# Performance work log

Hardware: AMD Instinct MI355X
Metric: run time of the kernel (lower is better)

Reference implementation:

```python
import jax, jax.numpy as jnp
import numpy as np

L, N, E, D = 4, 50000, 250000, 128
EPS = 1e-5

def _ln(h, g, b):
    mu = jnp.mean(h, axis=-1, keepdims=True)
    var = jnp.mean(jnp.square(h - mu), axis=-1, keepdims=True)
    return (h - mu) * jax.lax.rsqrt(var + EPS) * g + b

def setup_inputs() -> dict:
    key = jax.random.key(0)
    ks = jax.random.split(key, 8)
    s1 = 1.0 / np.sqrt(3 * D)
    s2 = 1.0 / np.sqrt(D)
    s3 = 1.0 / np.sqrt(2 * D)
    return {
        "x": jax.random.normal(ks[0], (N, D), jnp.float32),
        "edge_index": jax.random.randint(ks[1], (2, E), 0, N, jnp.int32),
        "edge_attr": jax.random.normal(ks[2], (E, D), jnp.float32),
        "eW1": jax.random.normal(ks[3], (L, 3 * D, D), jnp.float32) * s1,
        "eb1": jnp.zeros((L, D), jnp.float32),
        "eW2": jax.random.normal(ks[4], (L, D, D), jnp.float32) * s2,
        "eb2": jnp.zeros((L, D), jnp.float32),
        "eG": jnp.ones((L, D), jnp.float32),
        "eB": jnp.zeros((L, D), jnp.float32),
        "nW1": jax.random.normal(ks[5], (L, 2 * D, D), jnp.float32) * s3,
        "nb1": jnp.zeros((L, D), jnp.float32),
        "nW2": jax.random.normal(ks[6], (L, D, D), jnp.float32) * s2,
        "nb2": jnp.zeros((L, D), jnp.float32),
        "nG": jnp.ones((L, D), jnp.float32),
        "nB": jnp.zeros((L, D), jnp.float32),
    }

def reference(x, edge_index, edge_attr, eW1, eb1, eW2, eb2, eG, eB,
              nW1, nb1, nW2, nb2, nG, nB):
    src = edge_index[0]  # scatter target (custom aggregate uses edge_index[0])
    dst = edge_index[1]  # x_i under PyG source_to_target flow
    n_nodes = x.shape[0]

    def step(carry, p):
        xc, ea = carry
        ew1, eb1_, ew2, eb2_, eg, ebt, nw1, nb1_, nw2, nb2_, ng, nbt = p
        # message: cat(x_i, x_j, edge_attr) -> MLP -> residual
        m = jnp.concatenate([xc[dst], xc[src], ea], axis=1)  # [E, 3D]
        h = jax.nn.relu(m @ ew1 + eb1_) @ ew2 + eb2_
        ea_new = ea + _ln(h, eg, ebt)
        # aggregate: scatter-sum edges into nodes by edge_index[0]
        agg = jax.ops.segment_sum(ea_new, src, num_segments=n_nodes)  # [N, D]
        # update: cat(x, agg) -> MLP -> residual
        u = jnp.concatenate([xc, agg], axis=1)  # [N, 2D]
        h2 = jax.nn.relu(u @ nw1 + nb1_) @ nw2 + nb2_
        x_new = xc + _ln(h2, ng, nbt)
        return (x_new, ea_new), None

    (x_out, ea_out), _ = jax.lax.scan(
        step, (x, edge_attr),
        (eW1, eb1, eW2, eb2, eG, eB, nW1, nb1, nW2, nb2, nG, nB))
    return x_out, ea_out
```

## Files before the change

### kernel.cpp

```cpp
#include <hip/hip_runtime.h>
#include <hip/hip_bf16.h>

#define N_NODES 50000
#define N_EDGES 250000
#define DIM 128
#define LAYERS 4
#define LN_EPS 1e-5f

typedef __hip_bfloat16 bf16;
typedef float f32x4 __attribute__((ext_vector_type(4)));
typedef __bf16 bfx8 __attribute__((ext_vector_type(8)));
typedef unsigned short u16x8 __attribute__((ext_vector_type(8)));
typedef unsigned short u16x4 __attribute__((ext_vector_type(4)));
typedef unsigned int   u32x4 __attribute__((ext_vector_type(4)));

#define F_X   0
#define F_EA  1
#define F_EW1 2
#define F_EW2 3
#define F_EG  4
#define F_NW1 5
#define F_NW2 6
#define F_NG  7

__device__ __forceinline__ float b2f(bf16 v) { return __bfloat162float(v); }
__device__ __forceinline__ bf16  f2b(float v) { return __float2bfloat16(v); }
__device__ __forceinline__ unsigned short f2us(float v) {
    return __builtin_bit_cast(unsigned short, __float2bfloat16(v));
}
__device__ __forceinline__ float us2f(unsigned short u) {
    return __builtin_bit_cast(float, (unsigned)u << 16);
}

__device__ __forceinline__ float ldv(const void* p, size_t i, int f) {
    if (f) return ((const float*)p)[i];
    else   return b2f(((const bf16*)p)[i]);
}
__device__ __forceinline__ void stv(void* p, size_t i, float v, int f) {
    if (f) ((float*)p)[i] = v;
    else   ((bf16*)p)[i] = f2b(v);
}

__device__ __forceinline__ bfx8 cvt8(f32x4 lo, f32x4 hi) {
    u16x8 u;
    #pragma unroll
    for (int i = 0; i < 4; i++) { u[i] = f2us(lo[i]); u[i + 4] = f2us(hi[i]); }
    return __builtin_bit_cast(bfx8, u);
}

__device__ __forceinline__ void mfma8(const bf16* pBk, bfx8 a, f32x4* acc) {
    #pragma unroll
    for (int f = 0; f < 8; f++) {
        bfx8 b = *reinterpret_cast<const bfx8*>(pBk + f * 128);
        acc[f] = __builtin_amdgcn_mfma_f32_16x16x32_bf16(a, b, acc[f], 0, 0, 0);
    }
}

__global__ void k_detect(const void* x, const void* ea,
                         const void* eW1, const void* eW2,
                         const void* nW1, const void* nW2,
                         const void* eG, const void* nG,
                         int* flags)
{
    __shared__ int bad[6];
    const void* ptrs[6] = { x, ea, eW1, eW2, nW1, nW2 };
    const int t = threadIdx.x;
    if (t < 6) bad[t] = 0;
    __syncthreads();
    for (int b = 0; b < 6; b++) {
        const bf16* p = (const bf16*)ptrs[b];
        int isbad = 0;
        for (int i = t; i < 4096; i += 256) {
            float v = b2f(p[i]);
            if (!(fabsf(v) < 1e4f)) isbad = 1;
        }
        if (isbad) atomicOr(&bad[b], 1);
    }
    __syncthreads();
    if (t == 0) {
        flags[F_X]   = bad[0];
        flags[F_EA]  = bad[1];
        flags[F_EW1] = bad[2];
        flags[F_EW2] = bad[3];
        flags[F_NW1] = bad[4];
        flags[F_NW2] = bad[5];
        const bf16* g1 = (const bf16*)eG;
        const bf16* g2 = (const bf16*)nG;
        flags[F_EG] = (b2f(g1[0]) == 1.0f && b2f(g1[1]) == 1.0f) ? 0 : 1;
        flags[F_NG] = (b2f(g2[0]) == 1.0f && b2f(g2[1]) == 1.0f) ? 0 : 1;
    }
}

__global__ void k_init_x(const void* __restrict__ x_in, float* __restrict__ xf,
                         bf16* __restrict__ xb, const int* __restrict__ flags) {
    const int f = flags[F_X];
    size_t i = ((size_t)blockIdx.x * 256 + threadIdx.x) * 4;
    if (i >= (size_t)N_NODES * DIM) return;
    f32x4 v;
    if (f) {
        v = *(const f32x4*)((const float*)x_in + i);
    } else {
        u16x4 u = *(const u16x4*)((const unsigned short*)x_in + i);
        #pragma unroll
        for (int q = 0; q < 4; q++) v[q] = us2f(u[q]);
    }
    *(f32x4*)(xf + i) = v;
    u16x4 ub;
    #pragma unroll
    for (int q = 0; q < 4; q++) ub[q] = f2us(v[q]);
    *(u16x4*)((unsigned short*)xb + i) = ub;
}

__global__ void k_init_ea(const void* __restrict__ ea_in, void* __restrict__ d_out,
                          const int* __restrict__ flags) {
    const int fe = flags[F_EA];
    const int fo = flags[F_X];
    size_t i = ((size_t)blockIdx.x * 256 + threadIdx.x) * 4;
    if (i >= (size_t)N_EDGES * DIM) return;
    if (fe == fo) {
        if (fo) {
            float* d = (float*)d_out + (size_t)N_NODES * DIM;
            *(u32x4*)(d + i) = *(const u32x4*)((const float*)ea_in + i);
        } else {
            bf16* d = (bf16*)d_out + (size_t)N_NODES * DIM;
            *(u16x4*)((unsigned short*)d + i) =
                *(const u16x4*)((const unsigned short*)ea_in + i);
        }
    } else {
        f32x4 v;
        if (fe) v = *(const f32x4*)((const float*)ea_in + i);
        else {
            u16x4 u = *(const u16x4*)((const unsigned short*)ea_in + i);
            #pragma unroll
            for (int q = 0; q < 4; q++) v[q] = us2f(u[q]);
        }
        if (fo) {
            float* d = (float*)d_out + (size_t)N_NODES * DIM;
            *(f32x4*)(d + i) = v;
        } else {
            bf16* d = (bf16*)d_out + (size_t)N_NODES * DIM;
            u16x4 ub;
            #pragma unroll
            for (int q = 0; q < 4; q++) ub[q] = f2us(v[q]);
            *(u16x4*)((unsigned short*)d + i) = ub;
        }
    }
}

__global__ void k_wprep(const void* __restrict__ W, bf16* __restrict__ Wb,
                        int K, const int* __restrict__ flags, int fidx)
{
    const int f = flags[fidx];
    size_t i = (size_t)blockIdx.x * 256 + threadIdx.x;
    const int per = K * DIM;
    if (i >= (size_t)LAYERS * per) return;
    int l   = (int)(i / per);
    int rem = (int)(i % per);
    int j   = rem & 7;
    int c   = (rem >> 3) & 127;
    int kq  = rem >> 10;
    int k   = kq * 8 + j;
    Wb[i] = f2b(ldv(W, (size_t)l * per + (size_t)k * DIM + c, f));
}

__global__ void k_deg(const int* __restrict__ srcI, int* __restrict__ deg) {
    int e = blockIdx.x * 256 + threadIdx.x;
    if (e < N_EDGES) atomicAdd(&deg[srcI[e]], 1);
}

#define SCH ((N_NODES + 255) / 256)
__global__ void k_scan(const int* __restrict__ deg, int* __restrict__ off,
                       int* __restrict__ cur) {
    __shared__ int part[256];
    const int t = threadIdx.x;
    const int lo = t * SCH;
    const int hi = (lo + SCH < N_NODES) ? (lo + SCH) : N_NODES;
    int s = 0;
    for (int i = lo; i < hi; i++) s += deg[i];
    part[t] = s;
    __syncthreads();
    if (t == 0) {
        int run = 0;
        for (int i = 0; i < 256; i++) { int v = part[i]; part[i] = run; run += v; }
    }
    __syncthreads();
    int run = part[t];
    for (int i = lo; i < hi; i++) { off[i] = run; cur[i] = run; run += deg[i]; }
    if (hi == N_NODES) off[N_NODES] = run;
}

__global__ void k_fill(const int* __restrict__ srcI, int* __restrict__ cur,
                       int* __restrict__ lst) {
    int e = blockIdx.x * 256 + threadIdx.x;
    if (e < N_EDGES) {
        int p = atomicAdd(&cur[srcI[e]], 1);
        lst[p] = e;
    }
}

__global__ __launch_bounds__(256)
void k_edge(const bf16* __restrict__ xb,
            void* __restrict__ d_out,
            const int* __restrict__ srcI, const int* __restrict__ dstI,
            const bf16* __restrict__ W1b, const bf16* __restrict__ W2b,
            const void* __restrict__ b1, const void* __restrict__ b2,
            const void* __restrict__ G,  const void* __restrict__ B,
            const int* __restrict__ flags, int layer)
{
    __shared__ alignas(16) float smem[4][16 * 132];

    const int fo = flags[F_X];
    const int fg = flags[F_EG];

    void* ea = fo ? (void*)((float*)d_out + (size_t)N_NODES * DIM)
                  : (void*)((bf16*)d_out + (size_t)N_NODES * DIM);

    const bf16* W1l = W1b + (size_t)layer * 3 * DIM * DIM;
    const bf16* W2l = W2b + (size_t)layer * DIM * DIM;
    const bf16* b1l = (const bf16*)b1 + (size_t)layer * DIM;
    const bf16* b2l = (const bf16*)b2 + (size_t)layer * DIM;
    const bf16* Bl  = (const bf16*)B  + (size_t)layer * DIM;
    const void* Gl  = fg ? (const void*)((const float*)G + (size_t)layer * DIM)
                         : (const void*)((const bf16*)G  + (size_t)layer * DIM);

    const int tid  = threadIdx.x;
    const int wv   = tid >> 6;
    const int lane = tid & 63;
    const int cl   = lane & 15;
    const int kp   = lane >> 4;

    const int e0w = blockIdx.x * 64 + wv * 16;
    const int eA  = (e0w + cl < N_EDGES) ? (e0w + cl) : (N_EDGES - 1);
    const bf16* pAd = xb + (size_t)dstI[eA] * DIM + kp * 8;
    const bf16* pAs = xb + (size_t)srcI[eA] * DIM + kp * 8;
    const bf16* pB  = W1l + kp * 1024 + cl * 8;

    f32x4 acc[8];
    #pragma unroll
    for (int f = 0; f < 8; f++) acc[f] = (f32x4){0.f, 0.f, 0.f, 0.f};

    #pragma unroll
    for (int kk = 0; kk < 4; kk++)
        mfma8(pB + (size_t)kk * 4096,
              *reinterpret_cast<const bfx8*>(pAd + kk * 32), acc);
    #pragma unroll
    for (int kk = 0; kk < 4; kk++)
        mfma8(pB + (size_t)(kk + 4) * 4096,
              *reinterpret_cast<const bfx8*>(pAs + kk * 32), acc);
    if (fo) {
        const float* pAe = (const float*)ea + (size_t)eA * DIM + kp * 8;
        #pragma unroll
        for (int kk = 0; kk < 4; kk++) {
            f32x4 lo = *reinterpret_cast<const f32x4*>(pAe + kk * 32);
            f32x4 hi = *reinterpret_cast<const f32x4*>(pAe + kk * 32 + 4);
            mfma8(pB + (size_t)(kk + 8) * 4096, cvt8(lo, hi), acc);
        }
    } else {
        const bf16* pAe = (const bf16*)ea + (size_t)eA * DIM + kp * 8;
        #pragma unroll
        for (int kk = 0; kk < 4; kk++)
            mfma8(pB + (size_t)(kk + 8) * 4096,
                  *reinterpret_cast<const bfx8*>(pAe + kk * 32), acc);
    }

    char* hb = (char*)&smem[wv][0];
    #pragma unroll
    for (int f = 0; f < 8; f++) {
        const int col = f * 16 + cl;
        const float bias1 = b2f(b1l[col]);
        #pragma unroll
        for (int j = 0; j < 4; j++) {
            const int r = kp * 4 + j;
            float hv = fmaxf(acc[f][j] + bias1, 0.f);
            *(bf16*)(hb + r * 256 + ((col * 2) ^ ((r & 7) << 4))) = f2b(hv);
        }
    }

    const bf16* pB2 = W2l + kp * 1024 + cl * 8;
    f32x4 acc2[8];
    #pragma unroll
    for (int f = 0; f < 8; f++) acc2[f] = (f32x4){0.f, 0.f, 0.f, 0.f};
    #pragma unroll
    for (int kk = 0; kk < 4; kk++) {
        bfx8 a = *reinterpret_cast<const bfx8*>(
            hb + cl * 256 + ((kk * 64 + kp * 16) ^ ((cl & 7) << 4)));
        mfma8(pB2 + (size_t)kk * 4096, a, acc2);
    }

    float g_[8], be_[8];
    #pragma unroll
    for (int f = 0; f < 8; f++) {
        const int col = f * 16 + cl;
        const float bias2 = b2f(b2l[col]);
        #pragma unroll
        for (int j = 0; j < 4; j++) acc2[f][j] += bias2;
        g_[f]  = ldv(Gl, col, fg);
        be_[f] = b2f(Bl[col]);
    }
    float mu[4], rs[4];
    #pragma unroll
    for (int j = 0; j < 4; j++) {
        float s = 0.f, q = 0.f;
        #pragma unroll
        for (int f = 0; f < 8; f++) { float v = acc2[f][j]; s += v; q += v * v; }
        #pragma unroll
        for (int m = 1; m <= 8; m <<= 1) { s += __shfl_xor(s, m); q += __shfl_xor(q, m); }
        mu[j] = s * (1.f / DIM);
        float var = q * (1.f / DIM) - mu[j] * mu[j];
        rs[j] = rsqrtf(var + LN_EPS);
    }

    float* vs = &smem[wv][0];
    #pragma unroll
    for (int f = 0; f < 8; f++) {
        #pragma unroll
        for (int j = 0; j < 4; j++) {
            const float val = (acc2[f][j] - mu[j]) * rs[j] * g_[f] + be_[f];
            vs[(kp * 4 + j) * 132 + f * 16 + cl] = val;
        }
    }
    const int lr = lane >> 5;
    const int lc = (lane & 31) * 4;
    #pragma unroll
    for (int i = 0; i < 8; i++) {
        const int r2 = 2 * i + lr;
        const int e  = e0w + r2;
        if (e >= N_EDGES) continue;
        f32x4 v = *(const f32x4*)&vs[r2 * 132 + lc];
        const size_t off = (size_t)e * DIM + lc;
        if (fo) {
            float* pe = (float*)ea + off;
            f32x4 o = *(const f32x4*)pe;
            *(f32x4*)pe = o + v;
        } else {
            bf16* pe = (bf16*)ea + off;
            u16x4 uo = *(const u16x4*)(unsigned short*)pe;
            u16x4 un;
            #pragma unroll
            for (int q = 0; q < 4; q++) un[q] = f2us(us2f(uo[q]) + v[q]);
            *(u16x4*)(unsigned short*)pe = un;
        }
    }
}

__global__ __launch_bounds__(256)
void k_node(float* __restrict__ xf, bf16* __restrict__ xb,
            void* __restrict__ d_out,
            const int* __restrict__ off_, const int* __restrict__ lst,
            const bf16* __restrict__ W1b, const bf16* __restrict__ W2b,
            const void* __restrict__ b1, const void* __restrict__ b2,
            const void* __restrict__ G,  const void* __restrict__ B,
            const int* __restrict__ flags, int layer)
{
    __shared__ alignas(16) float smem[4][16 * 132];

    const int fo = flags[F_X];
    const int fg = flags[F_NG];

    const bf16* W1l = W1b + (size_t)layer * 2 * DIM * DIM;
    const bf16* W2l = W2b + (size_t)layer * DIM * DIM;
    const bf16* b1l = (const bf16*)b1 + (size_t)layer * DIM;
    const bf16* b2l = (const bf16*)b2 + (size_t)layer * DIM;
    const bf16* Bl  = (const bf16*)B  + (size_t)layer * DIM;
    const void* Gl  = fg ? (const void*)((const float*)G + (size_t)layer * DIM)
                         : (const void*)((const bf16*)G  + (size_t)layer * DIM);

    const int tid  = threadIdx.x;
    const int wv   = tid >> 6;
    const int lane = tid & 63;
    const int cl   = lane & 15;
    const int kp   = lane >> 4;

    const int n0w = blockIdx.x * 64 + wv * 16;
    const int nA  = (n0w + cl < N_NODES) ? (n0w + cl) : (N_NODES - 1);

    f32x4 agl[4], agh[4];
    #pragma unroll
    for (int kk = 0; kk < 4; kk++) {
        agl[kk] = (f32x4){0.f, 0.f, 0.f, 0.f};
        agh[kk] = (f32x4){0.f, 0.f, 0.f, 0.f};
    }
    {
        const int beg = off_[nA], end = off_[nA + 1];
        if (fo) {
            const float* base = (const float*)d_out + (size_t)N_NODES * DIM;
            for (int idx = beg; idx < end; ++idx) {
                const int e = lst[idx];
                const float* p = base + (size_t)e * DIM + kp * 8;
                #pragma unroll
                for (int kk = 0; kk < 4; kk++) {
                    agl[kk] += *(const f32x4*)(p + kk * 32);
                    agh[kk] += *(const f32x4*)(p + kk * 32 + 4);
                }
            }
        } else {
            const bf16* base = (const bf16*)d_out + (size_t)N_NODES * DIM;
            for (int idx = beg; idx < end; ++idx) {
                const int e = lst[idx];
                const bf16* p = base + (size_t)e * DIM + kp * 8;
                #pragma unroll
                for (int kk = 0; kk < 4; kk++) {
                    u16x8 u = *(const u16x8*)(const unsigned short*)(p + kk * 32);
                    #pragma unroll
                    for (int q = 0; q < 4; q++) {
                        agl[kk][q] += us2f(u[q]);
                        agh[kk][q] += us2f(u[q + 4]);
                    }
                }
            }
        }
    }

    const bf16* pAx = xb + (size_t)nA * DIM + kp * 8;
    const bf16* pB  = W1l + kp * 1024 + cl * 8;

    f32x4 acc[8];
    #pragma unroll
    for (int f = 0; f < 8; f++) acc[f] = (f32x4){0.f, 0.f, 0.f, 0.f};

    #pragma unroll
    for (int kk = 0; kk < 4; kk++)
        mfma8(pB + (size_t)kk * 4096,
              *reinterpret_cast<const bfx8*>(pAx + kk * 32), acc);
    #pragma unroll
    for (int kk = 0; kk < 4; kk++)
        mfma8(pB + (size_t)(kk + 4) * 4096, cvt8(agl[kk], agh[kk]), acc);

    char* hb = (char*)&smem[wv][0];
    #pragma unroll
    for (int f = 0; f < 8; f++) {
        const int col = f * 16 + cl;
        const float bias1 = b2f(b1l[col]);
        #pragma unroll
        for (int j = 0; j < 4; j++) {
            const int r = kp * 4 + j;
            float hv = fmaxf(acc[f][j] + bias1, 0.f);
            *(bf16*)(hb + r * 256 + ((col * 2) ^ ((r & 7) << 4))) = f2b(hv);
        }
    }

    const bf16* pB2 = W2l + kp * 1024 + cl * 8;
    f32x4 acc2[8];
    #pragma unroll
    for (int f = 0; f < 8; f++) acc2[f] = (f32x4){0.f, 0.f, 0.f, 0.f};
    #pragma unroll
    for (int kk = 0; kk < 4; kk++) {
        bfx8 a = *reinterpret_cast<const bfx8*>(
            hb + cl * 256 + ((kk * 64 + kp * 16) ^ ((cl & 7) << 4)));
        mfma8(pB2 + (size_t)kk * 4096, a, acc2);
    }

    float g_[8], be_[8];
    #pragma unroll
    for (int f = 0; f < 8; f++) {
        const int col = f * 16 + cl;
        const float bias2 = b2f(b2l[col]);
        #pragma unroll
        for (int j = 0; j < 4; j++) acc2[f][j] += bias2;
        g_[f]  = ldv(Gl, col, fg);
        be_[f] = b2f(Bl[col]);
    }
    float mu[4], rs[4];
    #pragma unroll
    for (int j = 0; j < 4; j++) {
        float s = 0.f, q = 0.f;
        #pragma unroll
        for (int f = 0; f < 8; f++) { float v = acc2[f][j]; s += v; q += v * v; }
        #pragma unroll
        for (int m = 1; m <= 8; m <<= 1) { s += __shfl_xor(s, m); q += __shfl_xor(q, m); }
        mu[j] = s * (1.f / DIM);
        float var = q * (1.f / DIM) - mu[j] * mu[j];
        rs[j] = rsqrtf(var + LN_EPS);
    }

    float* vs = &smem[wv][0];
    #pragma unroll
    for (int f = 0; f < 8; f++) {
        #pragma unroll
        for (int j = 0; j < 4; j++) {
            const float val = (acc2[f][j] - mu[j]) * rs[j] * g_[f] + be_[f];
            vs[(kp * 4 + j) * 132 + f * 16 + cl] = val;
        }
    }
    const bool wout = (layer == LAYERS - 1);
    const int lr = lane >> 5;
    const int lc = (lane & 31) * 4;
    #pragma unroll
    for (int i = 0; i < 8; i++) {
        const int r2 = 2 * i + lr;
        const int n2 = n0w + r2;
        if (n2 >= N_NODES) continue;
        f32x4 v = *(const f32x4*)&vs[r2 * 132 + lc];
        const size_t off = (size_t)n2 * DIM + lc;
        f32x4 xo = *(const f32x4*)&xf[off];
        f32x4 xn = xo + v;
        *(f32x4*)&xf[off] = xn;
        u16x4 ub;
        #pragma unroll
        for (int q = 0; q < 4; q++) ub[q] = f2us(xn[q]);
        *(u16x4*)((unsigned short*)xb + off) = ub;
        if (wout) {
            if (fo) *(f32x4*)((float*)d_out + off) = xn;
            else    *(u16x4*)((unsigned short*)(bf16*)d_out + off) = ub;
        }
    }
}

extern "C" void kernel_launch(void* const* d_in, const int* in_sizes, int n_in,
                              void* d_out, int out_size, void* d_ws, size_t ws_size,
                              hipStream_t stream)
{
    (void)in_sizes; (void)n_in; (void)out_size; (void)ws_size;
    const void* x_in  = d_in[0];
    const int*  ei    = (const int*)d_in[1];
    const void* ea_in = d_in[2];
    const void* eW1 = d_in[3];  const void* eb1 = d_in[4];
    const void* eW2 = d_in[5];  const void* eb2 = d_in[6];
    const void* eG  = d_in[7];  const void* eB  = d_in[8];
    const void* nW1 = d_in[9];  const void* nb1 = d_in[10];
    const void* nW2 = d_in[11]; const void* nb2 = d_in[12];
    const void* nG  = d_in[13]; const void* nB  = d_in[14];

    char* ws = (char*)d_ws;
    int* flags = (int*)ws;
    char* p = ws + 256;
    float* xf  = (float*)p;  p += (size_t)N_NODES * DIM * 4;
    bf16*  xb  = (bf16*)p;   p += (size_t)N_NODES * DIM * 2;
    bf16*  eW1b = (bf16*)p;  p += (size_t)LAYERS * 3 * DIM * DIM * 2;
    bf16*  eW2b = (bf16*)p;  p += (size_t)LAYERS * DIM * DIM * 2;
    bf16*  nW1b = (bf16*)p;  p += (size_t)LAYERS * 2 * DIM * DIM * 2;
    bf16*  nW2b = (bf16*)p;  p += (size_t)LAYERS * DIM * DIM * 2;
    int* deg     = (int*)p;  p += 200000;
    int* csr_off = (int*)p;  p += 200016;
    int* cur     = (int*)p;  p += 200000;
    int* lst     = (int*)p;  p += 1000000;

    const int* srcI = ei;
    const int* dstI = ei + N_EDGES;

    k_detect<<<1, 256, 0, stream>>>(x_in, ea_in, eW1, eW2, nW1, nW2, eG, nG, flags);
    k_init_x<<<(N_NODES * DIM / 4 + 255) / 256, 256, 0, stream>>>(x_in, xf, xb, flags);
    k_init_ea<<<(int)(((size_t)N_EDGES * DIM / 4 + 255) / 256), 256, 0, stream>>>(ea_in, d_out, flags);
    k_wprep<<<(LAYERS * 3 * DIM * DIM + 255) / 256, 256, 0, stream>>>(eW1, eW1b, 3 * DIM, flags, F_EW1);
    k_wprep<<<(LAYERS * DIM * DIM + 255) / 256, 256, 0, stream>>>(eW2, eW2b, DIM, flags, F_EW2);
    k_wprep<<<(LAYERS * 2 * DIM * DIM + 255) / 256, 256, 0, stream>>>(nW1, nW1b, 2 * DIM, flags, F_NW1);
    k_wprep<<<(LAYERS * DIM * DIM + 255) / 256, 256, 0, stream>>>(nW2, nW2b, DIM, flags, F_NW2);

    hipMemsetAsync(deg, 0, N_NODES * sizeof(int), stream);
    k_deg<<<(N_EDGES + 255) / 256, 256, 0, stream>>>(srcI, deg);
    k_scan<<<1, 256, 0, stream>>>(deg, csr_off, cur);
    k_fill<<<(N_EDGES + 255) / 256, 256, 0, stream>>>(srcI, cur, lst);

    for (int l = 0; l < LAYERS; l++) {
        k_edge<<<(N_EDGES + 63) / 64, 256, 0, stream>>>(
            xb, d_out, srcI, dstI, eW1b, eW2b, eb1, eb2, eG, eB, flags, l);
        k_node<<<(N_NODES + 63) / 64, 256, 0, stream>>>(
            xf, xb, d_out, csr_off, lst, nW1b, nW2b, nb1, nb2, nG, nB, flags, l);
    }
}
```

Baseline: 1.392 ms.

## Stage edge MLP weights in LDS and double edge block size

The edge kernel now copies the layer's full bf16 W1 and W2 (128 KB) into shared memory once per block. Each wave then reads its MFMA B operands from LDS instead of global memory or L2. The block grows to 512 threads covering 128 edges, and the per-wave scratch areas reuse the W1 region after a barrier. The aim is to cut repeated weight traffic from L2, at the cost of occupancy (about one block per CU because of LDS size), extra barriers, and possible LDS bank conflicts. The edge-attribute init kernel also drops its same-format copy fast path.

```diff
diff --git a/kernel.cpp b/kernel.cpp
--- a/kernel.cpp
+++ b/kernel.cpp
@@ -12,7 +12,6 @@
 typedef __bf16 bfx8 __attribute__((ext_vector_type(8)));
 typedef unsigned short u16x8 __attribute__((ext_vector_type(8)));
 typedef unsigned short u16x4 __attribute__((ext_vector_type(4)));
-typedef unsigned int   u32x4 __attribute__((ext_vector_type(4)));
 
 #define F_X   0
 #define F_EA  1
@@ -35,10 +34,6 @@
 __device__ __forceinline__ float ldv(const void* p, size_t i, int f) {
     if (f) return ((const float*)p)[i];
     else   return b2f(((const bf16*)p)[i]);
-}
-__device__ __forceinline__ void stv(void* p, size_t i, float v, int f) {
-    if (f) ((float*)p)[i] = v;
-    else   ((bf16*)p)[i] = f2b(v);
 }
 
 __device__ __forceinline__ bfx8 cvt8(f32x4 lo, f32x4 hi) {
@@ -117,33 +112,22 @@
     const int fo = flags[F_X];
     size_t i = ((size_t)blockIdx.x * 256 + threadIdx.x) * 4;
     if (i >= (size_t)N_EDGES * DIM) return;
-    if (fe == fo) {
-        if (fo) {
-            float* d = (float*)d_out + (size_t)N_NODES * DIM;
-            *(u32x4*)(d + i) = *(const u32x4*)((const float*)ea_in + i);
-        } else {
-            bf16* d = (bf16*)d_out + (size_t)N_NODES * DIM;
-            *(u16x4*)((unsigned short*)d + i) =
-                *(const u16x4*)((const unsigned short*)ea_in + i);
-        }
+    f32x4 v;
+    if (fe) v = *(const f32x4*)((const float*)ea_in + i);
+    else {
+        u16x4 u = *(const u16x4*)((const unsigned short*)ea_in + i);
+        #pragma unroll
+        for (int q = 0; q < 4; q++) v[q] = us2f(u[q]);
+    }
+    if (fo) {
+        float* d = (float*)d_out + (size_t)N_NODES * DIM;
+        *(f32x4*)(d + i) = v;
     } else {
-        f32x4 v;
-        if (fe) v = *(const f32x4*)((const float*)ea_in + i);
-        else {
-            u16x4 u = *(const u16x4*)((const unsigned short*)ea_in + i);
-            #pragma unroll
-            for (int q = 0; q < 4; q++) v[q] = us2f(u[q]);
-        }
-        if (fo) {
-            float* d = (float*)d_out + (size_t)N_NODES * DIM;
-            *(f32x4*)(d + i) = v;
-        } else {
-            bf16* d = (bf16*)d_out + (size_t)N_NODES * DIM;
-            u16x4 ub;
-            #pragma unroll
-            for (int q = 0; q < 4; q++) ub[q] = f2us(v[q]);
-            *(u16x4*)((unsigned short*)d + i) = ub;
-        }
+        bf16* d = (bf16*)d_out + (size_t)N_NODES * DIM;
+        u16x4 ub;
+        #pragma unroll
+        for (int q = 0; q < 4; q++) ub[q] = f2us(v[q]);
+        *(u16x4*)((unsigned short*)d + i) = ub;
     }
 }
 
@@ -198,7 +182,7 @@
     }
 }
 
-__global__ __launch_bounds__(256)
+__global__ __launch_bounds__(512)
 void k_edge(const bf16* __restrict__ xb,
             void* __restrict__ d_out,
             const int* __restrict__ srcI, const int* __restrict__ dstI,
@@ -207,7 +191,7 @@
             const void* __restrict__ G,  const void* __restrict__ B,
             const int* __restrict__ flags, int layer)
 {
-    __shared__ alignas(16) float smem[4][16 * 132];
+    __shared__ alignas(16) float smem[32768];
 
     const int fo = flags[F_X];
     const int fg = flags[F_EG];
@@ -229,11 +213,23 @@
     const int cl   = lane & 15;
     const int kp   = lane >> 4;
 
-    const int e0w = blockIdx.x * 64 + wv * 16;
+    {
+        f32x4* dst = (f32x4*)smem;
+        const f32x4* s1 = (const f32x4*)W1l;
+        const f32x4* s2 = (const f32x4*)W2l;
+        #pragma unroll
+        for (int r = 0; r < 12; r++) dst[tid + r * 512] = s1[tid + r * 512];
+        #pragma unroll
+        for (int r = 0; r < 4; r++)  dst[6144 + tid + r * 512] = s2[tid + r * 512];
+    }
+    __syncthreads();
+
+    const int e0w = blockIdx.x * 128 + wv * 16;
     const int eA  = (e0w + cl < N_EDGES) ? (e0w + cl) : (N_EDGES - 1);
     const bf16* pAd = xb + (size_t)dstI[eA] * DIM + kp * 8;
     const bf16* pAs = xb + (size_t)srcI[eA] * DIM + kp * 8;
-    const bf16* pB  = W1l + kp * 1024 + cl * 8;
+    const bf16* pWl = (const bf16*)smem;
+    const bf16* pB  = pWl + kp * 1024 + cl * 8;
 
     f32x4 acc[8];
     #pragma unroll
@@ -262,8 +258,9 @@
             mfma8(pB + (size_t)(kk + 8) * 4096,
                   *reinterpret_cast<const bfx8*>(pAe + kk * 32), acc);
     }
-
-    char* hb = (char*)&smem[wv][0];
+    __syncthreads();
+
+    char* hb = (char*)smem + wv * 4224;
     #pragma unroll
     for (int f = 0; f < 8; f++) {
         const int col = f * 16 + cl;
@@ -276,7 +273,7 @@
         }
     }
 
-    const bf16* pB2 = W2l + kp * 1024 + cl * 8;
+    const bf16* pB2 = (const bf16*)smem + 49152 + kp * 1024 + cl * 8;
     f32x4 acc2[8];
     #pragma unroll
     for (int f = 0; f < 8; f++) acc2[f] = (f32x4){0.f, 0.f, 0.f, 0.f};
@@ -309,8 +306,9 @@
         float var = q * (1.f / DIM) - mu[j] * mu[j];
         rs[j] = rsqrtf(var + LN_EPS);
     }
-
-    float* vs = &smem[wv][0];
+    __syncthreads();
+
+    float* vs = smem + wv * 2112;
     #pragma unroll
     for (int f = 0; f < 8; f++) {
         #pragma unroll
@@ -552,7 +550,7 @@
     k_fill<<<(N_EDGES + 255) / 256, 256, 0, stream>>>(srcI, cur, lst);
 
     for (int l = 0; l < LAYERS; l++) {
-        k_edge<<<(N_EDGES + 63) / 64, 256, 0, stream>>>(
+        k_edge<<<(N_EDGES + 127) / 128, 512, 0, stream>>>(
             xb, d_out, srcI, dstI, eW1b, eW2b, eb1, eb2, eG, eB, flags, l);
         k_node<<<(N_NODES + 63) / 64, 256, 0, stream>>>(
             xf, xb, d_out, csr_off, lst, nW1b, nW2b, nb1, nb2, nG, nB, flags, l);
```

Measured after the change: 1.290 ms. 7.3% less time.
